# Kernel tuning notes

Hardware: AMD Instinct MI355X
Metric: run time of the kernel (lower is better)

Reference implementation:

```python
import jax, jax.numpy as jnp
import numpy as np

CLASS_W, MASK_W, DICE_W = 1.0, 1.0, 1.0
BIG = 1.0e6


def _hungarian_np(cost):
    """Jonker-Volgenant style shortest-augmenting-path Hungarian (same optimum as
    scipy.optimize.linear_sum_assignment). cost: [R, C] numpy. Returns (row_ind, col_ind)
    with row_ind sorted ascending."""
    C = np.asarray(cost, dtype=np.float64)
    transposed = C.shape[0] > C.shape[1]
    if transposed:
        C = C.T
    n, m = C.shape  # n <= m
    u = np.zeros(n + 1)
    v = np.zeros(m + 1)
    p = np.zeros(m + 1, dtype=np.int64)   # p[j] = row (1-based) matched to col j
    way = np.zeros(m + 1, dtype=np.int64)
    for i in range(1, n + 1):
        p[0] = i
        j0 = 0
        minv = np.full(m + 1, np.inf)
        used = np.zeros(m + 1, dtype=bool)
        while True:
            used[j0] = True
            i0 = p[j0]
            free = ~used
            free[0] = False
            js = np.nonzero(free)[0]
            cur = C[i0 - 1, js - 1] - u[i0] - v[js]
            upd = cur < minv[js]
            minv[js] = np.where(upd, cur, minv[js])
            way[js] = np.where(upd, j0, way[js])
            j1 = js[np.argmin(minv[js])]
            delta = minv[j1]
            u[p[used]] += delta
            v[used] -= delta
            minv[free] -= delta
            j0 = j1
            if p[j0] == 0:
                break
        while j0 != 0:
            j1 = way[j0]
            p[j0] = p[j1]
            j0 = j1
    cols = np.nonzero(p[1:])[0]
    rows = p[1:][cols] - 1
    if transposed:
        rows, cols = cols, rows
    order = np.argsort(rows)
    return rows[order], cols[order]


def _cost_matrix(pred_logits, pred_masks, target_masks, target_labels):
    B, N, H, W = pred_masks.shape
    T = target_labels.shape[1]
    HW = H * W
    # classification cost: -softmax(logits)[..., :-1][:, labels]
    out_prob = jax.nn.softmax(pred_logits, axis=-1)[..., :-1]          # [B, N, C]
    onehot = jax.nn.one_hot(target_labels, out_prob.shape[-1], dtype=out_prob.dtype)  # [B, T, C]
    cost_class = -jnp.einsum('bnc,btc->bnt', out_prob, onehot)
    # nearest-neighbor resize of target masks to pred mask resolution (torch F.interpolate 'nearest')
    Ht, Wt = target_masks.shape[-2:]
    ri = (jnp.arange(H) * Ht) // H
    ci = (jnp.arange(W) * Wt) // W
    tm = target_masks[:, :, ri][:, :, :, ci].reshape(B, T, HW)          # [B, T, HW]
    pm = pred_masks.reshape(B, N, HW)                                    # [B, N, HW]
    # sigmoid BCE cost (vs all-ones/all-zeros decomposition)
    cost_mask = jax.nn.softplus(pm).mean(-1)[:, :, None] - jnp.einsum('bnp,btp->bnt', pm, tm) / HW
    # dice cost
    ps = jax.nn.sigmoid(pm)
    numerator = 2.0 * jnp.einsum('bnp,btp->bnt', ps, tm)
    denominator = ps.sum(-1)[:, :, None] + tm.sum(-1)[:, None, :]
    cost_dice = 1.0 - (numerator + 1.0) / (denominator + 1.0)
    cost = CLASS_W * cost_class + MASK_W * cost_mask + DICE_W * cost_dice
    return jnp.nan_to_num(cost, nan=BIG, posinf=BIG, neginf=-BIG)       # [B, N, T]


_cost_matrix_jit = jax.jit(_cost_matrix)


def setup_inputs() -> dict:
    key = jax.random.key(0)
    k1, k2, k3, k4 = jax.random.split(key, 4)
    pred_logits = jax.random.normal(k1, (8, 100, 81), dtype=jnp.float32)
    pred_masks = jax.random.normal(k2, (8, 100, 256, 256), dtype=jnp.float32)
    target_masks = (jax.random.uniform(k3, (8, 32, 512, 512)) < 0.3).astype(jnp.float32)
    target_labels = jax.random.randint(k4, (8, 32), 0, 80)
    return {
        'pred_logits': pred_logits,
        'pred_masks': pred_masks,
        'target_masks': target_masks,
        'target_labels': target_labels,
    }


def reference(pred_logits, pred_masks, target_masks, target_labels):
    cost = _cost_matrix_jit(pred_logits, pred_masks, target_masks, target_labels)
    costs = np.asarray(cost)  # host sync, mirrors the original .cpu() round-trip
    src_list, tgt_list = [], []
    for b in range(costs.shape[0]):  # serial per-image assignment (inherent to Hungarian)
        r, c = _hungarian_np(costs[b])
        src_list.append(r)
        tgt_list.append(c)
    src = jnp.asarray(np.stack(src_list), dtype=jnp.int64)  # [B, T] query indices
    tgt = jnp.asarray(np.stack(tgt_list), dtype=jnp.int64)  # [B, T] target indices
    return (src, tgt)
```

## Files before the change

### kernel.cpp

```cpp
#include <hip/hip_runtime.h>
#include <stdint.h>


#define BATCH 8
#define NQ    100
#define NT    32
#define HWP   65536
#define NCLS  81
#define BIGV  1.0e6
#define MPAD  112
#define MTILES 7
#define KSPLIT 16
#define KC (HWP / KSPLIT)
#define KW (KC / 4)
#define NITER (KW / 64)

typedef __attribute__((ext_vector_type(8))) short short8;
typedef __attribute__((ext_vector_type(4))) float f32x4;

union FragU { short8 s; uint32_t w[4]; };

__device__ inline uint32_t cvt_pk_bf16(float lo, float hi) {
    uint32_t r;
    asm("v_cvt_pk_bf16_f32 %0, %1, %2" : "=v"(r) : "v"(lo), "v"(hi));
    return r;
}

__device__ inline void bpair(uint32_t wlo, uint32_t whi, int r,
                             uint32_t& lofrag, uint32_t& hifrag) {
    uint32_t a = wlo >> r;
    uint32_t c = whi >> r;
    lofrag = ((a & 1u) | ((c & 1u) << 16)) * 0x3F80u;
    hifrag = (((a >> 16) & 1u) | (((c >> 16) & 1u) << 16)) * 0x3F80u;
}

__global__ __launch_bounds__(256) void pack_kernel(const float* __restrict__ tmask,
                                                   uint32_t* __restrict__ packed,
                                                   int* __restrict__ tm_counts) {
    int idx = blockIdx.x * 256 + threadIdx.x;
    int b  = idx >> 15;
    int pp = idx & 32767;
    int y  = pp >> 7;
    int xp = pp & 127;
    const float* base = tmask + (size_t)b * NT * 262144 + (size_t)(2 * y) * 512 + 4 * xp;
    uint32_t w0 = 0, w1 = 0;
#pragma unroll
    for (int t = 0; t < NT; ++t) {
        float4 v = *(const float4*)(base + (size_t)t * 262144);
        w0 |= (v.x > 0.5f ? 1u : 0u) << t;
        w1 |= (v.z > 0.5f ? 1u : 0u) << t;
    }
    int p0 = y * 256 + 2 * xp;
    *(uint2*)(packed + (size_t)b * HWP + p0) = make_uint2(w0, w1);

    int lane = threadIdx.x & 63;
    int mycnt = 0;
#pragma unroll
    for (int t = 0; t < NT; ++t) {
        unsigned long long m0 = __ballot((w0 >> t) & 1u);
        unsigned long long m1 = __ballot((w1 >> t) & 1u);
        if (lane == t) mycnt = __popcll(m0) + __popcll(m1);
    }
    if (lane < NT) atomicAdd(&tm_counts[b * NT + lane], mycnt);
}

__global__ __launch_bounds__(256) void mfma_kernel(const float* __restrict__ pmask,
                                                   const uint32_t* __restrict__ packed,
                                                   float* __restrict__ accd,
                                                   float* __restrict__ accs) {
    const int kblk = blockIdx.x;
    const int mt   = blockIdx.y;
    const int b    = blockIdx.z;
    const int tid  = threadIdx.x;
    const int wv   = tid >> 6, lane = tid & 63;
    const int m0   = mt * 16;
    const int q    = lane >> 4;
    const int r    = lane & 15;

    __shared__ float Cred[8][16][32];

    int mrow = m0 + r; if (mrow > NQ - 1) mrow = NQ - 1;
    const float* Arow = pmask + (size_t)b * NQ * HWP + (size_t)mrow * HWP;
    const uint32_t* pkb = packed + (size_t)b * HWP;
    const int kbase0 = kblk * KC + wv * KW;

    f32x4 Cpm0 = {0,0,0,0}, Cpm1 = {0,0,0,0}, Csg0 = {0,0,0,0}, Csg1 = {0,0,0,0};
    float rsp = 0.f, rsg = 0.f;

    for (int ki = 0; ki < NITER; ++ki) {
        const int kb = kbase0 + ki * 64;
        const float4 va0 = *(const float4*)(Arow + kb + q * 8);
        const float4 va1 = *(const float4*)(Arow + kb + q * 8 + 4);
        const float4 va2 = *(const float4*)(Arow + kb + 32 + q * 8);
        const float4 va3 = *(const float4*)(Arow + kb + 32 + q * 8 + 4);
        const uint4  wb0 = *(const uint4*)(pkb + kb + q * 8);
        const uint4  wb1 = *(const uint4*)(pkb + kb + q * 8 + 4);
        const uint4  wb2 = *(const uint4*)(pkb + kb + 32 + q * 8);
        const uint4  wb3 = *(const uint4*)(pkb + kb + 32 + q * 8 + 4);

        FragU a0, a1, g0, g1;
        auto proc4 = [&](const float4& v, uint32_t* aw, uint32_t* gw) {
            float sg[4];
#pragma unroll
            for (int e = 0; e < 4; ++e) {
                float pv = (&v.x)[e];
                float ax = fabsf(pv);
                float en = __expf(-ax);
                float one_en = 1.0f + en;
                float inv = __builtin_amdgcn_rcpf(one_en);
                float sig = (pv >= 0.f) ? inv : en * inv;
                float sp  = fmaxf(pv, 0.f) + __logf(one_en);
                rsp += sp; rsg += sig;
                sg[e] = sig;
            }
            aw[0] = cvt_pk_bf16(v.x, v.y);
            aw[1] = cvt_pk_bf16(v.z, v.w);
            gw[0] = cvt_pk_bf16(sg[0], sg[1]);
            gw[1] = cvt_pk_bf16(sg[2], sg[3]);
        };
        proc4(va0, &a0.w[0], &g0.w[0]);
        proc4(va1, &a0.w[2], &g0.w[2]);
        proc4(va2, &a1.w[0], &g1.w[0]);
        proc4(va3, &a1.w[2], &g1.w[2]);

        FragU b00, b01, b10, b11;
        bpair(wb0.x, wb0.y, r, b00.w[0], b10.w[0]);
        bpair(wb0.z, wb0.w, r, b00.w[1], b10.w[1]);
        bpair(wb1.x, wb1.y, r, b00.w[2], b10.w[2]);
        bpair(wb1.z, wb1.w, r, b00.w[3], b10.w[3]);
        bpair(wb2.x, wb2.y, r, b01.w[0], b11.w[0]);
        bpair(wb2.z, wb2.w, r, b01.w[1], b11.w[1]);
        bpair(wb3.x, wb3.y, r, b01.w[2], b11.w[2]);
        bpair(wb3.z, wb3.w, r, b01.w[3], b11.w[3]);

        Cpm0 = __builtin_amdgcn_mfma_f32_16x16x32_bf16(a0.s, b00.s, Cpm0, 0, 0, 0);
        Cpm0 = __builtin_amdgcn_mfma_f32_16x16x32_bf16(a1.s, b01.s, Cpm0, 0, 0, 0);
        Cpm1 = __builtin_amdgcn_mfma_f32_16x16x32_bf16(a0.s, b10.s, Cpm1, 0, 0, 0);
        Cpm1 = __builtin_amdgcn_mfma_f32_16x16x32_bf16(a1.s, b11.s, Cpm1, 0, 0, 0);
        Csg0 = __builtin_amdgcn_mfma_f32_16x16x32_bf16(g0.s, b00.s, Csg0, 0, 0, 0);
        Csg0 = __builtin_amdgcn_mfma_f32_16x16x32_bf16(g1.s, b01.s, Csg0, 0, 0, 0);
        Csg1 = __builtin_amdgcn_mfma_f32_16x16x32_bf16(g0.s, b10.s, Csg1, 0, 0, 0);
        Csg1 = __builtin_amdgcn_mfma_f32_16x16x32_bf16(g1.s, b11.s, Csg1, 0, 0, 0);
    }

    rsp += __shfl_xor(rsp, 16, 64);
    rsp += __shfl_xor(rsp, 32, 64);
    rsg += __shfl_xor(rsg, 16, 64);
    rsg += __shfl_xor(rsg, 32, 64);
    if (q == 0 && m0 + r < NQ) {
        atomicAdd(&accs[(size_t)b * MPAD + m0 + r], rsp);
        atomicAdd(&accs[(size_t)(BATCH + b) * MPAD + m0 + r], rsg);
    }

#pragma unroll
    for (int e = 0; e < 4; ++e) {
        const int m = q * 4 + e;
        Cred[wv * 2 + 0][m][r]      = Cpm0[e];
        Cred[wv * 2 + 0][m][16 + r] = Cpm1[e];
        Cred[wv * 2 + 1][m][r]      = Csg0[e];
        Cred[wv * 2 + 1][m][16 + r] = Csg1[e];
    }
    __syncthreads();
    for (int idx = tid; idx < 1024; idx += 256) {
        const int type = idx >> 9, rem = idx & 511, m = rem >> 5, n = rem & 31;
        float s = Cred[0 + type][m][n] + Cred[2 + type][m][n]
                + Cred[4 + type][m][n] + Cred[6 + type][m][n];
        const int gm = m0 + m;
        if (gm < NQ)
            atomicAdd(&accd[(size_t)(type * BATCH + b) * MPAD * 32 + (size_t)gm * 32 + n], s);
    }
}

__global__ __launch_bounds__(64) void hungarian_kernel(const float* __restrict__ logits,
                                                       const int* __restrict__ labels,
                                                       const float* __restrict__ accd,
                                                       const float* __restrict__ accs,
                                                       const int* __restrict__ tm_counts,
                                                       int* __restrict__ out) {
    const int b = blockIdx.x;
    const int lane = threadIdx.x;

    __shared__ double Ct[NT][NQ];
    __shared__ double u[NT + 1];
    __shared__ float smx[NQ], ssm[NQ];
    __shared__ float tcs[NT];
    __shared__ int lab[NT];

    if (lane < NT) { tcs[lane] = (float)tm_counts[b * NT + lane]; lab[lane] = labels[b * NT + lane]; }
    for (int n = lane; n < NQ; n += 64) {
        const float* lg = logits + (size_t)(b * NQ + n) * NCLS;
        float mx = -1e30f;
        for (int c = 0; c < NCLS; ++c) mx = fmaxf(mx, lg[c]);
        float s = 0.f;
        for (int c = 0; c < NCLS; ++c) s += __expf(lg[c] - mx);
        smx[n] = mx; ssm[n] = s;
    }
    if (lane <= NT) u[lane] = 0.0;
    __syncthreads();
    for (int idx = lane; idx < NQ * NT; idx += 64) {
        const int t2 = idx & 31, q2 = idx >> 5;
        float dpm = accd[(size_t)b * MPAD * 32 + q2 * 32 + t2];
        float dsg = accd[(size_t)(BATCH + b) * MPAD * 32 + q2 * 32 + t2];
        float ssp = accs[(size_t)b * MPAD + q2];
        float ssg = accs[(size_t)(BATCH + b) * MPAD + q2];
        float lg = logits[(size_t)(b * NQ + q2) * NCLS + lab[t2]];
        float prob = __expf(lg - smx[q2]) / ssm[q2];
        float c = -prob + (ssp - dpm) * (1.0f / (float)HWP)
                + 1.0f - (2.0f * dsg + 1.0f) / (ssg + tcs[t2] + 1.0f);
        if (isnan(c)) c = (float)BIGV;
        else if (isinf(c)) c = (c > 0.f) ? (float)BIGV : -(float)BIGV;
        Ct[t2][q2] = (double)c;
    }
    __syncthreads();

    const int c0 = lane + 1;
    const bool valid1 = (lane < NQ - 64);
    const int c1 = lane + 65;
    const int cidx1 = valid1 ? (lane + 64) : 0;

    double v0 = 0.0, v1 = 0.0;
    int p0 = 0, p1 = 0;
    double u_reg = 0.0;

    for (int i = 1; i <= NT; ++i) {
        double minv0 = 1e300, minv1 = 1e300;
        int way0 = 0, way1 = 0;
        bool used0 = false, used1 = !valid1;
        double du0 = 0.0, du1 = 0.0, dtot = 0.0;
        int j0 = 0, i0 = i;
        int jfin = 0;

        for (int guard = 0; guard < 160; ++guard) {
            double u_i0 = __shfl(u_reg, i0, 64);
            double cur0 = Ct[i0 - 1][lane] - u_i0 - v0;
            if (!used0 && cur0 < minv0) { minv0 = cur0; way0 = j0; }
            double cur1 = Ct[i0 - 1][cidx1] - u_i0 - v1;
            if (!used1 && cur1 < minv1) { minv1 = cur1; way1 = j0; }
            double bv = 1e301; int bj = 1 << 20;
            if (!used0) { bv = minv0; bj = c0; }
            if (!used1 && minv1 < bv) { bv = minv1; bj = c1; }
#pragma unroll
            for (int s = 32; s > 0; s >>= 1) {
                double ov = __shfl_down(bv, s, 64);
                int    oj = __shfl_down(bj, s, 64);
                if (ov < bv || (ov == bv && oj < bj)) { bv = ov; bj = oj; }
            }
            double delta = __shfl(bv, 0, 64);
            int j1 = __shfl(bj, 0, 64);
            dtot += delta;
            if (used0) { v0 -= delta; du0 += delta; } else { minv0 -= delta; }
            if (valid1) {
                if (used1) { v1 -= delta; du1 += delta; } else { minv1 -= delta; }
            }
            if (c0 == j1) used0 = true;
            if (valid1 && c1 == j1) used1 = true;
            int src = (j1 - 1) & 63, slot = (j1 - 1) >> 6;
            int pa = __shfl(p0, src, 64), pb = __shfl(p1, src, 64);
            int pj1 = slot ? pb : pa;
            if (pj1 == 0) { jfin = j1; break; }
            j0 = j1; i0 = pj1;
        }

        if (used0 && p0 != 0) u[p0] += du0;
        if (valid1 && used1 && p1 != 0) u[p1] += du1;
        if (lane == 0) u[i] += dtot;

        int jj = jfin;
        for (int guard = 0; guard < 160 && jj != 0; ++guard) {
            int src = (jj - 1) & 63, slot = (jj - 1) >> 6;
            int wa = __shfl(way0, src, 64), wb = __shfl(way1, src, 64);
            int jprev = slot ? wb : wa;
            int pnew;
            if (jprev == 0) pnew = i;
            else {
                int s2 = (jprev - 1) & 63, sl2 = (jprev - 1) >> 6;
                int pa = __shfl(p0, s2, 64), pb = __shfl(p1, s2, 64);
                pnew = sl2 ? pb : pa;
            }
            if (c0 == jj) p0 = pnew;
            if (valid1 && c1 == jj) p1 = pnew;
            jj = jprev;
        }
        __syncthreads();
        u_reg = (lane <= NT) ? u[lane] : 0.0;
    }

    unsigned long long m0 = __ballot(p0 != 0);
    unsigned long long m1 = __ballot(valid1 && p1 != 0);
    int base = b * NT;
    if (p0 != 0) {
        int rank = __popcll(m0 & ((1ull << lane) - 1ull));
        out[base + rank] = c0 - 1;
        out[BATCH * NT + base + rank] = p0 - 1;
    }
    if (valid1 && p1 != 0) {
        int rank = __popcll(m0) + __popcll(m1 & ((1ull << lane) - 1ull));
        out[base + rank] = c1 - 1;
        out[BATCH * NT + base + rank] = p1 - 1;
    }
}

extern "C" void kernel_launch(void* const* d_in, const int* in_sizes, int n_in,
                              void* d_out, int out_size, void* d_ws, size_t ws_size,
                              hipStream_t stream) {
    const float* logits = (const float*)d_in[0];
    const float* pmasks = (const float*)d_in[1];
    const float* tmasks = (const float*)d_in[2];
    const int*   labels = (const int*)d_in[3];

    uint8_t* ws = (uint8_t*)d_ws;
    uint32_t* packed = (uint32_t*)ws;
    uint8_t* zbase = ws + (size_t)BATCH * HWP * 4;
    int* tm_counts = (int*)zbase;
    float* accd = (float*)(zbase + 1024);
    float* accs = (float*)(zbase + 1024 + 229376);
    const size_t ztotal = 1024 + 229376 + 7168;

    int* out = (int*)d_out;

    hipMemsetAsync(zbase, 0, ztotal, stream);
    pack_kernel<<<BATCH * HWP / 512, 256, 0, stream>>>(tmasks, packed, tm_counts);
    mfma_kernel<<<dim3(KSPLIT, MTILES, BATCH), 256, 0, stream>>>(pmasks, packed, accd, accs);
    hungarian_kernel<<<BATCH, 64, 0, stream>>>(logits, labels, accd, accs, tm_counts, out);
}
```

Baseline: 590.7 us.

## Compute target mask counts via MFMA ones row and fold zeroing into pack kernel

Target pixel counts are no longer computed with per-wave ballots and atomics in the pack kernel. Instead, padded query row 100 of the MFMA tile has its A fragment set to bf16 ones, so the dot-product accumulator for that row yields the per-target counts for free. The separate hipMemsetAsync is replaced by having the pack kernel zero the accumulation buffers, which removes one launch, and the bf16 one-hot multiply becomes shifts. Relying on pack_kernel finishing its zeroing before mfma_kernel's atomics depends on stream ordering. The counts now pass through a bf16 MFMA with fp32 accumulation, which is exact for counts of this size.

After: 590.8 us. Within noise of the previous version (+0.0%).

```diff
diff --git a/kernel.cpp b/kernel.cpp
--- a/kernel.cpp
+++ b/kernel.cpp
@@ -14,6 +14,7 @@
 #define KC (HWP / KSPLIT)
 #define KW (KC / 4)
 #define NITER (KW / 64)
+#define NZFLOAT 59136
 
 typedef __attribute__((ext_vector_type(8))) short short8;
 typedef __attribute__((ext_vector_type(4))) float f32x4;
@@ -30,14 +31,17 @@
                              uint32_t& lofrag, uint32_t& hifrag) {
     uint32_t a = wlo >> r;
     uint32_t c = whi >> r;
-    lofrag = ((a & 1u) | ((c & 1u) << 16)) * 0x3F80u;
-    hifrag = (((a >> 16) & 1u) | (((c >> 16) & 1u) << 16)) * 0x3F80u;
+    uint32_t mlo = (a & 1u) | ((c & 1u) << 16);
+    uint32_t mhi = ((a >> 16) & 1u) | (((c >> 16) & 1u) << 16);
+    lofrag = (mlo << 14) - (mlo << 7);
+    hifrag = (mhi << 14) - (mhi << 7);
 }
 
 __global__ __launch_bounds__(256) void pack_kernel(const float* __restrict__ tmask,
                                                    uint32_t* __restrict__ packed,
-                                                   int* __restrict__ tm_counts) {
+                                                   float* __restrict__ zbuf) {
     int idx = blockIdx.x * 256 + threadIdx.x;
+    if (idx < NZFLOAT) zbuf[idx] = 0.f;
     int b  = idx >> 15;
     int pp = idx & 32767;
     int y  = pp >> 7;
@@ -52,16 +56,6 @@
     }
     int p0 = y * 256 + 2 * xp;
     *(uint2*)(packed + (size_t)b * HWP + p0) = make_uint2(w0, w1);
-
-    int lane = threadIdx.x & 63;
-    int mycnt = 0;
-#pragma unroll
-    for (int t = 0; t < NT; ++t) {
-        unsigned long long m0 = __ballot((w0 >> t) & 1u);
-        unsigned long long m1 = __ballot((w1 >> t) & 1u);
-        if (lane == t) mycnt = __popcll(m0) + __popcll(m1);
-    }
-    if (lane < NT) atomicAdd(&tm_counts[b * NT + lane], mycnt);
 }
 
 __global__ __launch_bounds__(256) void mfma_kernel(const float* __restrict__ pmask,
@@ -79,6 +73,7 @@
 
     __shared__ float Cred[8][16][32];
 
+    const bool onesrow = (m0 + r == 100);
     int mrow = m0 + r; if (mrow > NQ - 1) mrow = NQ - 1;
     const float* Arow = pmask + (size_t)b * NQ * HWP + (size_t)mrow * HWP;
     const uint32_t* pkb = packed + (size_t)b * HWP;
@@ -123,6 +118,11 @@
         proc4(va2, &a1.w[0], &g1.w[0]);
         proc4(va3, &a1.w[2], &g1.w[2]);
 
+        if (onesrow) {
+#pragma unroll
+            for (int i2 = 0; i2 < 4; ++i2) { a0.w[i2] = 0x3F803F80u; a1.w[i2] = 0x3F803F80u; }
+        }
+
         FragU b00, b01, b10, b11;
         bpair(wb0.x, wb0.y, r, b00.w[0], b10.w[0]);
         bpair(wb0.z, wb0.w, r, b00.w[1], b10.w[1]);
@@ -166,7 +166,7 @@
         float s = Cred[0 + type][m][n] + Cred[2 + type][m][n]
                 + Cred[4 + type][m][n] + Cred[6 + type][m][n];
         const int gm = m0 + m;
-        if (gm < NQ)
+        if (gm < 101)
             atomicAdd(&accd[(size_t)(type * BATCH + b) * MPAD * 32 + (size_t)gm * 32 + n], s);
     }
 }
@@ -175,7 +175,6 @@
                                                        const int* __restrict__ labels,
                                                        const float* __restrict__ accd,
                                                        const float* __restrict__ accs,
-                                                       const int* __restrict__ tm_counts,
                                                        int* __restrict__ out) {
     const int b = blockIdx.x;
     const int lane = threadIdx.x;
@@ -186,7 +185,10 @@
     __shared__ float tcs[NT];
     __shared__ int lab[NT];
 
-    if (lane < NT) { tcs[lane] = (float)tm_counts[b * NT + lane]; lab[lane] = labels[b * NT + lane]; }
+    if (lane < NT) {
+        tcs[lane] = accd[(size_t)b * MPAD * 32 + 100 * 32 + lane];
+        lab[lane] = labels[b * NT + lane];
+    }
     for (int n = lane; n < NQ; n += 64) {
         const float* lg = logits + (size_t)(b * NQ + n) * NCLS;
         float mx = -1e30f;
@@ -311,15 +313,12 @@
     uint8_t* ws = (uint8_t*)d_ws;
     uint32_t* packed = (uint32_t*)ws;
     uint8_t* zbase = ws + (size_t)BATCH * HWP * 4;
-    int* tm_counts = (int*)zbase;
-    float* accd = (float*)(zbase + 1024);
-    float* accs = (float*)(zbase + 1024 + 229376);
-    const size_t ztotal = 1024 + 229376 + 7168;
+    float* accd = (float*)zbase;
+    float* accs = (float*)(zbase + 229376);
 
     int* out = (int*)d_out;
 
-    hipMemsetAsync(zbase, 0, ztotal, stream);
-    pack_kernel<<<BATCH * HWP / 512, 256, 0, stream>>>(tmasks, packed, tm_counts);
+    pack_kernel<<<BATCH * HWP / 512, 256, 0, stream>>>(tmasks, packed, accd);
     mfma_kernel<<<dim3(KSPLIT, MTILES, BATCH), 256, 0, stream>>>(pmasks, packed, accd, accs);
-    hungarian_kernel<<<BATCH, 64, 0, stream>>>(logits, labels, accd, accs, tm_counts, out);
-}
+    hungarian_kernel<<<BATCH, 64, 0, stream>>>(logits, labels, accd, accs, out);
+}
```
